# Kernel tuning notes

Measured on AMD Instinct MI355X. Metric: run time of the kernel, lower is better.

## Reference

```python
import jax, jax.numpy as jnp
import numpy as np

A = 5.0  # smoothness parameter 'a'

def setup_inputs() -> dict:
    key = jax.random.key(0)
    kx, kw = jax.random.split(key)
    x = jax.random.uniform(kx, (1024, 512), dtype=jnp.float32)
    weight = jax.random.uniform(kw, (512, 512), dtype=jnp.float32)
    return {"x": x, "weight": weight}

def reference(x, weight):
    # inner: [batch, in, out] broadcast min
    inner = jnp.minimum(x[..., None], weight[None])
    # smooth union (smooth max) over the 'in' dim: logsumexp(a*z)/a
    smooth = jax.scipy.special.logsumexp(A * inner, axis=-2) / A
    hard = jnp.max(inner, axis=-2)
    # straight-through: forward value = hard, gradient flows through smooth
    return jax.lax.stop_gradient(hard - smooth) + smooth
```

## Files before the change

### kernel.cpp

```cpp
#include <hip/hip_runtime.h>
#include <float.h>


#define MDIM 1024
#define KDIM 512
#define NDIM 512
#define MB 8
#define NT 256
#define KW 64

__device__ __forceinline__ float bcast(float v, int srcLane) {
    return __int_as_float(__builtin_amdgcn_readlane(__float_as_int(v), srcLane));
}

__global__ __launch_bounds__(512) void tropical_rl(
    const float* __restrict__ x,
    const float* __restrict__ w,
    float* __restrict__ out)
{
    const int tid  = threadIdx.x;
    const int lane = tid & 63;
    const int wv   = tid >> 6;
    const int m0   = blockIdx.x * MB;
    const int n0   = blockIdx.y * NT;
    const int k0   = wv * KW;

    __shared__ float red[MB][NT];
    {
        float4* r4 = (float4*)&red[0][0];
        float4 z; z.x = z.y = z.z = z.w = 0.0f;
        r4[tid] = z;
    }

    float xreg[MB];
#pragma unroll
    for (int r = 0; r < MB; ++r)
        xreg[r] = x[(size_t)(m0 + r) * KDIM + k0 + lane];

#define WROW(kk) (((const float4*)(w + (size_t)(k0 + (kk)) * NDIM + n0))[lane])

    float acc[MB][4];
#pragma unroll
    for (int r = 0; r < MB; ++r)
#pragma unroll
        for (int j = 0; j < 4; ++j) acc[r][j] = 0.0f;

    float4 wA = WROW(0), wB = WROW(1);
    float4 wC = WROW(2), wD = WROW(3);

#pragma unroll 2
    for (int k = 0; k < KW; k += 2) {
        const int kp = (k + 4 < KW) ? (k + 4) : (KW - 2);
        float4 wE = WROW(kp), wF = WROW(kp + 1);

        float xb0[MB], xb1[MB];
#pragma unroll
        for (int r = 0; r < MB; ++r) {
            xb0[r] = bcast(xreg[r], k);
            xb1[r] = bcast(xreg[r], k + 1);
        }
#pragma unroll
        for (int r = 0; r < MB; ++r) {
            float a0 = acc[r][0], a1 = acc[r][1], a2 = acc[r][2], a3 = acc[r][3];
            a0 = fmaxf(fmaxf(a0, fminf(xb0[r], wA.x)), fminf(xb1[r], wB.x));
            a1 = fmaxf(fmaxf(a1, fminf(xb0[r], wA.y)), fminf(xb1[r], wB.y));
            a2 = fmaxf(fmaxf(a2, fminf(xb0[r], wA.z)), fminf(xb1[r], wB.z));
            a3 = fmaxf(fmaxf(a3, fminf(xb0[r], wA.w)), fminf(xb1[r], wB.w));
            acc[r][0] = a0; acc[r][1] = a1; acc[r][2] = a2; acc[r][3] = a3;
        }
        wA = wC; wB = wD; wC = wE; wD = wF;
    }
#undef WROW

    __syncthreads();

#pragma unroll
    for (int r = 0; r < MB; ++r)
#pragma unroll
        for (int j = 0; j < 4; ++j)
            atomicMax((unsigned int*)&red[r][4 * lane + j],
                      __float_as_uint(acc[r][j]));

    __syncthreads();

    {
        const int r  = tid >> 6;
        const int c4 = tid & 63;
        float4 v = ((const float4*)&red[r][0])[c4];
        *(float4*)(out + (size_t)(m0 + r) * NDIM + n0 + 4 * c4) = v;
    }
}

extern "C" void kernel_launch(void* const* d_in, const int* in_sizes, int n_in,
                              void* d_out, int out_size, void* d_ws, size_t ws_size,
                              hipStream_t stream) {
    const float* x = (const float*)d_in[0];
    const float* w = (const float*)d_in[1];
    float* out = (float*)d_out;

    dim3 grid(MDIM / MB, NDIM / NT);
    tropical_rl<<<grid, dim3(512), 0, stream>>>(x, w, out);
}
```

Measured before the change: 77.93 us.

## Replace LDS atomicMax reduction with per-wave buffers and tree max

Each wave now writes its partial max tile to its own LDS slice, and one pass of reads then reduces across the eight waves. This replaces 32 LDS atomicMax operations per thread and drops the zero-init. The weight prefetch is restructured into fully unrolled chunks of four rows, and launch bounds now request two blocks per CU. In exchange, LDS use grows eightfold to 64KB per block, which may limit occupancy despite the launch-bounds hint.

```diff
diff --git a/kernel.cpp b/kernel.cpp
--- a/kernel.cpp
+++ b/kernel.cpp
@@ -8,12 +8,13 @@
 #define MB 8
 #define NT 256
 #define KW 64
+#define NWAVE 8
 
-__device__ __forceinline__ float bcast(float v, int srcLane) {
+__device__ __forceinline__ float bcastc(float v, int srcLane) {
     return __int_as_float(__builtin_amdgcn_readlane(__float_as_int(v), srcLane));
 }
 
-__global__ __launch_bounds__(512) void tropical_rl(
+__global__ __launch_bounds__(512, 2) void tropical_r8(
     const float* __restrict__ x,
     const float* __restrict__ w,
     float* __restrict__ out)
@@ -25,19 +26,15 @@
     const int n0   = blockIdx.y * NT;
     const int k0   = wv * KW;
 
-    __shared__ float red[MB][NT];
-    {
-        float4* r4 = (float4*)&red[0][0];
-        float4 z; z.x = z.y = z.z = z.w = 0.0f;
-        r4[tid] = z;
-    }
+    __shared__ float red[NWAVE][MB][NT];
 
     float xreg[MB];
 #pragma unroll
     for (int r = 0; r < MB; ++r)
         xreg[r] = x[(size_t)(m0 + r) * KDIM + k0 + lane];
 
-#define WROW(kk) (((const float4*)(w + (size_t)(k0 + (kk)) * NDIM + n0))[lane])
+    const float4* __restrict__ wb =
+        (const float4*)(w + (size_t)k0 * NDIM + n0) + lane;
 
     float acc[MB][4];
 #pragma unroll
@@ -45,48 +42,59 @@
 #pragma unroll
         for (int j = 0; j < 4; ++j) acc[r][j] = 0.0f;
 
-    float4 wA = WROW(0), wB = WROW(1);
-    float4 wC = WROW(2), wD = WROW(3);
+    float4 cur0 = wb[0 * 128], cur1 = wb[1 * 128];
+    float4 cur2 = wb[2 * 128], cur3 = wb[3 * 128];
 
-#pragma unroll 2
-    for (int k = 0; k < KW; k += 2) {
-        const int kp = (k + 4 < KW) ? (k + 4) : (KW - 2);
-        float4 wE = WROW(kp), wF = WROW(kp + 1);
-
-        float xb0[MB], xb1[MB];
 #pragma unroll
-        for (int r = 0; r < MB; ++r) {
-            xb0[r] = bcast(xreg[r], k);
-            xb1[r] = bcast(xreg[r], k + 1);
+    for (int kc = 0; kc < KW; kc += 4) {
+        float4 nx0, nx1, nx2, nx3;
+        if (kc + 4 < KW) {
+            nx0 = wb[(kc + 4) * 128]; nx1 = wb[(kc + 5) * 128];
+            nx2 = wb[(kc + 6) * 128]; nx3 = wb[(kc + 7) * 128];
         }
 #pragma unroll
-        for (int r = 0; r < MB; ++r) {
-            float a0 = acc[r][0], a1 = acc[r][1], a2 = acc[r][2], a3 = acc[r][3];
-            a0 = fmaxf(fmaxf(a0, fminf(xb0[r], wA.x)), fminf(xb1[r], wB.x));
-            a1 = fmaxf(fmaxf(a1, fminf(xb0[r], wA.y)), fminf(xb1[r], wB.y));
-            a2 = fmaxf(fmaxf(a2, fminf(xb0[r], wA.z)), fminf(xb1[r], wB.z));
-            a3 = fmaxf(fmaxf(a3, fminf(xb0[r], wA.w)), fminf(xb1[r], wB.w));
-            acc[r][0] = a0; acc[r][1] = a1; acc[r][2] = a2; acc[r][3] = a3;
+        for (int p = 0; p < 2; ++p) {
+            const float4 wlo = p ? cur2 : cur0;
+            const float4 whi = p ? cur3 : cur1;
+            const int kk = kc + 2 * p;
+            float xb0[MB], xb1[MB];
+#pragma unroll
+            for (int r = 0; r < MB; ++r) {
+                xb0[r] = bcastc(xreg[r], kk);
+                xb1[r] = bcastc(xreg[r], kk + 1);
+            }
+#pragma unroll
+            for (int r = 0; r < MB; ++r) {
+                acc[r][0] = fmaxf(acc[r][0],
+                                  fmaxf(fminf(xb0[r], wlo.x), fminf(xb1[r], whi.x)));
+                acc[r][1] = fmaxf(acc[r][1],
+                                  fmaxf(fminf(xb0[r], wlo.y), fminf(xb1[r], whi.y)));
+                acc[r][2] = fmaxf(acc[r][2],
+                                  fmaxf(fminf(xb0[r], wlo.z), fminf(xb1[r], whi.z)));
+                acc[r][3] = fmaxf(acc[r][3],
+                                  fmaxf(fminf(xb0[r], wlo.w), fminf(xb1[r], whi.w)));
+            }
         }
-        wA = wC; wB = wD; wC = wE; wD = wF;
+        if (kc + 4 < KW) { cur0 = nx0; cur1 = nx1; cur2 = nx2; cur3 = nx3; }
     }
-#undef WROW
-
-    __syncthreads();
 
 #pragma unroll
-    for (int r = 0; r < MB; ++r)
-#pragma unroll
-        for (int j = 0; j < 4; ++j)
-            atomicMax((unsigned int*)&red[r][4 * lane + j],
-                      __float_as_uint(acc[r][j]));
-
+    for (int r = 0; r < MB; ++r) {
+        float4 v; v.x = acc[r][0]; v.y = acc[r][1]; v.z = acc[r][2]; v.w = acc[r][3];
+        ((float4*)&red[wv][r][0])[lane] = v;
+    }
     __syncthreads();
 
     {
         const int r  = tid >> 6;
         const int c4 = tid & 63;
-        float4 v = ((const float4*)&red[r][0])[c4];
+        float4 v = ((const float4*)&red[0][r][0])[c4];
+#pragma unroll
+        for (int q = 1; q < NWAVE; ++q) {
+            float4 u = ((const float4*)&red[q][r][0])[c4];
+            v.x = fmaxf(v.x, u.x); v.y = fmaxf(v.y, u.y);
+            v.z = fmaxf(v.z, u.z); v.w = fmaxf(v.w, u.w);
+        }
         *(float4*)(out + (size_t)(m0 + r) * NDIM + n0 + 4 * c4) = v;
     }
 }
@@ -99,5 +107,5 @@
     float* out = (float*)d_out;
 
     dim3 grid(MDIM / MB, NDIM / NT);
-    tropical_rl<<<grid, dim3(512), 0, stream>>>(x, w, out);
+    tropical_r8<<<grid, dim3(512), 0, stream>>>(x, w, out);
 }
```

New measurement: 189.4 us. 143% more time.
